# Kernel tuning notes

Measured on AMD Instinct MI355X. Metric: run time of the kernel, lower is better.

The kernel has to match this reference:

```python
import jax, jax.numpy as jnp
from jax import lax
import numpy as np

H_FEAT = 14
W_FEAT = 14
BN_EPS = 1e-5
NORM_EPS = 1e-12

def _coord_tensor():
    # Python-2 integer division as in the original repo
    c = np.zeros((H_FEAT * W_FEAT, 2), dtype=np.float32)
    for i in range(H_FEAT * W_FEAT):
        c[i, 0] = (i // W_FEAT - H_FEAT // 2) / (H_FEAT / 2.0)
        c[i, 1] = (i % W_FEAT - W_FEAT // 2) / (W_FEAT / 2.0)
    return jnp.asarray(c.reshape(1, H_FEAT, W_FEAT, 2).transpose(0, 3, 1, 2))  # [1,2,14,14]

def _l2norm(x, axis):
    n = jnp.linalg.norm(x, axis=axis, keepdims=True)
    return x / jnp.maximum(n, NORM_EPS)

def _conv2d(x, w, b, pad):
    y = lax.conv_general_dilated(x, w, (1, 1), [(pad, pad), (pad, pad)],
                                 dimension_numbers=("NCHW", "OIHW", "NCHW"))
    return y + b[None, :, None, None]

def _bn_train(x, g, b):
    m = x.mean(axis=(0, 2, 3), keepdims=True)
    v = x.var(axis=(0, 2, 3), keepdims=True)
    return (x - m) * lax.rsqrt(v + BN_EPS) * g[None, :, None, None] + b[None, :, None, None]

def _lstm_scan(emb, Wih, Whh, bih, bhh):
    # emb: [T, B, 300]; PyTorch gate order i,f,g,o
    Hdim = Whh.shape[1]
    B = emb.shape[1]
    def step(carry, x):
        h, c = carry
        gates = x @ Wih.T + h @ Whh.T + bih + bhh  # [B, 4H]
        i, f, g, o = jnp.split(gates, 4, axis=-1)
        c = jax.nn.sigmoid(f) * c + jax.nn.sigmoid(i) * jnp.tanh(g)
        h = jax.nn.sigmoid(o) * jnp.tanh(c)
        return (h, c), h
    init = (jnp.zeros((B, Hdim), emb.dtype), jnp.zeros((B, Hdim), emb.dtype))
    _, hs = lax.scan(step, init, emb)
    return hs  # [T, B, H]

def _resblock(v, coord, c1w, c1b, c2w, c2b, bng, bnb):
    B = v.shape[0]
    vin = jnp.concatenate([v, jnp.broadcast_to(coord, (B, 2, H_FEAT, W_FEAT))], axis=1)
    v1 = jax.nn.relu(_conv2d(vin, c1w, c1b, 0))
    v2 = jax.nn.relu(_bn_train(_conv2d(v1, c2w, c2b, 1), bng, bnb))
    return v2 + v1

def setup_inputs() -> dict:
    key = jax.random.key(0)
    ks = jax.random.split(key, 24)
    B, T, V, E = 128, 45, 10000, 300
    Hh = 1024
    s = 0.02
    inp = {}
    inp["que"] = jax.random.randint(ks[0], (B, T), 0, V, dtype=jnp.int64)
    inp["img"] = jax.random.normal(ks[1], (B, 1024, H_FEAT, W_FEAT), dtype=jnp.float32)
    inp["lookup"] = s * jax.random.normal(ks[2], (V + 1, E), dtype=jnp.float32)
    inp["Wih_f"] = s * jax.random.normal(ks[3], (4 * Hh, E), dtype=jnp.float32)
    inp["Whh_f"] = s * jax.random.normal(ks[4], (4 * Hh, Hh), dtype=jnp.float32)
    inp["bih_f"] = jnp.zeros((4 * Hh,), jnp.float32)
    inp["bhh_f"] = jnp.zeros((4 * Hh,), jnp.float32)
    inp["Wih_b"] = s * jax.random.normal(ks[5], (4 * Hh, E), dtype=jnp.float32)
    inp["Whh_b"] = s * jax.random.normal(ks[6], (4 * Hh, Hh), dtype=jnp.float32)
    inp["bih_b"] = jnp.zeros((4 * Hh,), jnp.float32)
    inp["bhh_b"] = jnp.zeros((4 * Hh,), jnp.float32)
    inp["conv0_w"] = s * jax.random.normal(ks[7], (128, 1026, 3, 3), dtype=jnp.float32)
    inp["conv0_b"] = jnp.zeros((128,), jnp.float32)
    inp["bn0_g"] = jnp.ones((128,), jnp.float32)
    inp["bn0_b"] = jnp.zeros((128,), jnp.float32)
    inp["r1c1_w"] = s * jax.random.normal(ks[8], (128, 130, 1, 1), dtype=jnp.float32)
    inp["r1c1_b"] = jnp.zeros((128,), jnp.float32)
    inp["r1c2_w"] = s * jax.random.normal(ks[9], (128, 128, 3, 3), dtype=jnp.float32)
    inp["r1c2_b"] = jnp.zeros((128,), jnp.float32)
    inp["r1bn_g"] = jnp.ones((128,), jnp.float32)
    inp["r1bn_b"] = jnp.zeros((128,), jnp.float32)
    inp["r2c1_w"] = s * jax.random.normal(ks[10], (128, 130, 1, 1), dtype=jnp.float32)
    inp["r2c1_b"] = jnp.zeros((128,), jnp.float32)
    inp["r2c2_w"] = s * jax.random.normal(ks[11], (128, 128, 3, 3), dtype=jnp.float32)
    inp["r2c2_b"] = jnp.zeros((128,), jnp.float32)
    inp["r2bn_g"] = jnp.ones((128,), jnp.float32)
    inp["r2bn_b"] = jnp.zeros((128,), jnp.float32)
    return inp

def reference(que, img, lookup, Wih_f, Whh_f, bih_f, bhh_f, Wih_b, Whh_b, bih_b, bhh_b,
              conv0_w, conv0_b, bn0_g, bn0_b,
              r1c1_w, r1c1_b, r1c2_w, r1c2_b, r1bn_g, r1bn_b,
              r2c1_w, r2c1_b, r2c2_w, r2c2_b, r2bn_g, r2bn_b):
    coord = _coord_tensor()
    # ---- encoder (LSTM mode) ----
    emb = lookup[que]                      # [B, T, 300]
    emb = jnp.transpose(emb, (1, 0, 2))    # [T, B, 300]
    h_f = _lstm_scan(emb, Wih_f, Whh_f, bih_f, bhh_f)
    h_b = _lstm_scan(emb[::-1], Wih_b, Whh_b, bih_b, bhh_b)[::-1]
    qenc = _l2norm(jnp.concatenate([h_f, h_b], axis=-1), axis=-1)  # [T, B, 2048]
    enc = qenc[-1]                                                  # [B, 2048]
    # ---- image branch ----
    v = _l2norm(img, axis=1)               # per-pixel L2 norm over 1024 channels
    B = v.shape[0]
    v = jnp.concatenate([v, jnp.broadcast_to(coord, (B, 2, H_FEAT, W_FEAT))], axis=1)
    v = jax.nn.relu(_bn_train(_conv2d(v, conv0_w, conv0_b, 1), bn0_g, bn0_b))
    v = _resblock(v, coord, r1c1_w, r1c1_b, r1c2_w, r1c2_b, r1bn_g, r1bn_b)
    v = _resblock(v, coord, r2c1_w, r2c1_b, r2c2_w, r2c2_b, r2bn_g, r2bn_b)
    return (enc, v)
```

## Files before the change

### kernel.cpp

```cpp
#include <hip/hip_runtime.h>
#include <math.h>

#define BB   128
#define T    45
#define E    300
#define HH   1024
#define G4   4096
#define HW   196
#define NPX  (BB*HW)
#define C0   1026
#define CM   128
#define CR   130
#define TCH  15

static __device__ __forceinline__ float sigm(float x) { return 1.f / (1.f + __expf(-x)); }

__global__ void k_embed(const int* __restrict__ que, const float* __restrict__ lookup,
                        float* __restrict__ emb) {
    int idx = blockIdx.x * 256 + threadIdx.x;
    if (idx >= T * BB * E) return;
    int e = idx % E;
    int n = idx / E;
    int b = n % BB;
    int t = n / BB;
    int q = que[b * T + t];
    emb[idx] = lookup[(size_t)q * E + e];
}

template <int BM, int BN, int TM, int TN>
__global__ __launch_bounds__(256) void k_gemm_nt(
    const float* __restrict__ A, int lda,
    const float* __restrict__ Bw, int ldb,
    const float* __restrict__ add,
    const float* __restrict__ bias,
    float* __restrict__ C, int ldc,
    int M, int N, int K, int relu) {
    constexpr int KT = 16;
    constexpr int TX = BN / TN;
    __shared__ alignas(16) float As[KT][BM + 4];
    __shared__ alignas(16) float Bs[KT][BN + 4];
    const int tid = threadIdx.x;
    const int tx = tid % TX, ty = tid / TX;
    const int r0 = blockIdx.x * BM, c0 = blockIdx.y * BN;
    float acc[TM][TN] = {};
    for (int k0 = 0; k0 < K; k0 += KT) {
#pragma unroll
        for (int l = tid; l < BM * KT; l += 256) {
            int m = l / KT, k = l % KT;
            int gm = r0 + m, gk = k0 + k;
            As[k][m] = (gm < M && gk < K) ? A[(size_t)gm * lda + gk] : 0.f;
        }
#pragma unroll
        for (int l = tid; l < BN * KT; l += 256) {
            int n = l / KT, k = l % KT;
            int gn = c0 + n, gk = k0 + k;
            Bs[k][n] = (gn < N && gk < K) ? Bw[(size_t)gn * ldb + gk] : 0.f;
        }
        __syncthreads();
#pragma unroll
        for (int k = 0; k < KT; ++k) {
            float ar[TM], br[TN];
            if constexpr ((TM & 3) == 0) {
#pragma unroll
                for (int i = 0; i < TM; i += 4) {
                    float4 v = *(const float4*)&As[k][ty * TM + i];
                    ar[i] = v.x; ar[i + 1] = v.y; ar[i + 2] = v.z; ar[i + 3] = v.w;
                }
            } else if constexpr ((TM & 1) == 0) {
#pragma unroll
                for (int i = 0; i < TM; i += 2) {
                    float2 v = *(const float2*)&As[k][ty * TM + i];
                    ar[i] = v.x; ar[i + 1] = v.y;
                }
            } else {
#pragma unroll
                for (int i = 0; i < TM; ++i) ar[i] = As[k][ty * TM + i];
            }
            if constexpr ((TN & 3) == 0) {
#pragma unroll
                for (int j = 0; j < TN; j += 4) {
                    float4 v = *(const float4*)&Bs[k][tx * TN + j];
                    br[j] = v.x; br[j + 1] = v.y; br[j + 2] = v.z; br[j + 3] = v.w;
                }
            } else if constexpr ((TN & 1) == 0) {
#pragma unroll
                for (int j = 0; j < TN; j += 2) {
                    float2 v = *(const float2*)&Bs[k][tx * TN + j];
                    br[j] = v.x; br[j + 1] = v.y;
                }
            } else {
#pragma unroll
                for (int j = 0; j < TN; ++j) br[j] = Bs[k][tx * TN + j];
            }
#pragma unroll
            for (int i = 0; i < TM; ++i)
#pragma unroll
                for (int j = 0; j < TN; ++j) acc[i][j] += ar[i] * br[j];
        }
        __syncthreads();
    }
#pragma unroll
    for (int i = 0; i < TM; ++i) {
        int gm = r0 + ty * TM + i;
        if (gm >= M) continue;
#pragma unroll
        for (int j = 0; j < TN; ++j) {
            int gn = c0 + tx * TN + j;
            if (gn >= N) continue;
            float v = acc[i][j];
            if (add) v += add[(size_t)gm * ldc + gn];
            if (bias) v += bias[gn];
            if (relu) v = fmaxf(v, 0.f);
            C[(size_t)gm * ldc + gn] = v;
        }
    }
}

__global__ void k_pack_wih(const float* __restrict__ Wih, float* __restrict__ o) {
    int idx = blockIdx.x * 256 + threadIdx.x;
    if (idx >= G4 * E) return;
    int k = idx % E;
    int n = idx / E;
    o[idx] = Wih[(size_t)((n & 3) * HH + (n >> 2)) * E + k];
}
__global__ void k_pack_whh(const float* __restrict__ Whh, float* __restrict__ o) {
    int idx = blockIdx.x * 256 + threadIdx.x;
    if (idx >= G4 * HH) return;
    int k = idx & 1023;
    int n = idx >> 10;
    o[idx] = Whh[(size_t)((n & 3) * HH + (n >> 2)) * HH + k];
}
__global__ void k_pack_b4i(const float* __restrict__ bih, const float* __restrict__ bhh,
                           float* __restrict__ out) {
    int n = blockIdx.x * 256 + threadIdx.x;
    if (n >= G4) return;
    int r = (n & 3) * HH + (n >> 2);
    out[n] = bih[r] + bhh[r];
}
__global__ void k_biasadd(const float* __restrict__ bih, const float* __restrict__ bhh,
                          float* __restrict__ out) {
    int idx = blockIdx.x * 256 + threadIdx.x;
    if (idx < G4) out[idx] = bih[idx] + bhh[idx];
}

__global__ void k_cell_plain(float* __restrict__ h, float* __restrict__ c,
                             const float* __restrict__ gx, int first) {
    int idx = blockIdx.x * 256 + threadIdx.x;
    int b = idx >> 10, j = idx & 1023;
    size_t base = (size_t)b * G4 + j;
    float gi = gx[base], gf = gx[base + HH], gg = gx[base + 2 * HH], go = gx[base + 3 * HH];
    float cp = first ? 0.f : c[idx];
    float cn = sigm(gf) * cp + sigm(gi) * tanhf(gg);
    c[idx] = cn;
    h[idx] = sigm(go) * tanhf(cn);
}

__global__ __launch_bounds__(256) void k_lstm_fused(
    const float* __restrict__ h_in, float* __restrict__ c_io,
    const float* __restrict__ gx,
    const float* __restrict__ Wpk,
    float* __restrict__ h_out, int first) {
    __shared__ alignas(16) float As[16][20];
    __shared__ alignas(16) float Bs[16][68];
    const int tid = threadIdx.x;
    const int tx = tid & 15, ty = tid >> 4;
    const int id = blockIdx.x;
    const int xcd = id & 7, slot = id >> 3;
    const int cg = xcd * 8 + (slot >> 3);
    const int rb = slot & 7;
    const int r0 = rb * 16;
    const int c0 = cg * 64;
    const int ka = tid & 15, ma = tid >> 4;
    float acc[4] = {};

    if (!first) {
        const float* hrow = h_in + (size_t)(r0 + ma) * HH + ka;
        const float* wp0 = Wpk + (size_t)(c0 + ma) * HH + ka;
        float aA = hrow[0];
        float b0A = wp0[0], b1A = wp0[16 * HH], b2A = wp0[32 * HH], b3A = wp0[48 * HH];
        float aB = hrow[16];
        float b0B = wp0[16], b1B = wp0[16 * HH + 16], b2B = wp0[32 * HH + 16],
              b3B = wp0[48 * HH + 16];
        for (int k0 = 0; k0 < HH; k0 += 16) {
            As[ka][ma] = aA;
            Bs[ka][ma] = b0A;
            Bs[ka][ma + 16] = b1A;
            Bs[ka][ma + 32] = b2A;
            Bs[ka][ma + 48] = b3A;
            __syncthreads();
            aA = aB; b0A = b0B; b1A = b1B; b2A = b2B; b3A = b3B;
            if (k0 + 32 < HH) {
                int o = k0 + 32;
                aB = hrow[o];
                b0B = wp0[o];
                b1B = wp0[16 * HH + o];
                b2B = wp0[32 * HH + o];
                b3B = wp0[48 * HH + o];
            }
#pragma unroll
            for (int k = 0; k < 16; ++k) {
                float a = As[k][ty];
                float4 b4 = *(const float4*)&Bs[k][tx * 4];
                acc[0] += a * b4.x;
                acc[1] += a * b4.y;
                acc[2] += a * b4.z;
                acc[3] += a * b4.w;
            }
            __syncthreads();
        }
    }
    const int b = r0 + ty;
    const int jj4 = c0 + tx * 4;
    const int u = jj4 >> 2;
    float4 g4 = *(const float4*)&gx[(size_t)b * G4 + jj4];
    float gi = acc[0] + g4.x;
    float gf = acc[1] + g4.y;
    float gg = acc[2] + g4.z;
    float go = acc[3] + g4.w;
    size_t ci = (size_t)b * HH + u;
    float cp = first ? 0.f : c_io[ci];
    float cn = sigm(gf) * cp + sigm(gi) * tanhf(gg);
    c_io[ci] = cn;
    h_out[ci] = sigm(go) * tanhf(cn);
}

__global__ void k_enc(const float* __restrict__ hf, const float* __restrict__ hb,
                      float* __restrict__ out) {
    int b = blockIdx.x;
    int tid = threadIdx.x;
    float vals[8];
    float ss = 0.f;
#pragma unroll
    for (int i = 0; i < 8; ++i) {
        int j = i * 256 + tid;
        float v = (j < HH) ? hf[(size_t)b * HH + j] : hb[(size_t)b * HH + (j - HH)];
        vals[i] = v;
        ss += v * v;
    }
    __shared__ float red[256];
    red[tid] = ss;
    __syncthreads();
    for (int s = 128; s > 0; s >>= 1) {
        if (tid < s) red[tid] += red[tid + s];
        __syncthreads();
    }
    float scale = 1.f / fmaxf(sqrtf(red[0]), 1e-12f);
#pragma unroll
    for (int i = 0; i < 8; ++i) out[(size_t)b * 2048 + i * 256 + tid] = vals[i] * scale;
}

__global__ void k_pixssq(const float* __restrict__ img, float* __restrict__ ssq) {
    int b = blockIdx.x >> 4;
    int cc = (blockIdx.x & 15) * 64;
    int p = threadIdx.x;
    if (p >= HW) return;
    const float* base = img + ((size_t)b * 1024 + cc) * HW + p;
    float acc = 0.f;
#pragma unroll 4
    for (int c = 0; c < 64; ++c) {
        float v = base[(size_t)c * HW];
        acc += v * v;
    }
    atomicAdd(&ssq[b * HW + p], acc);
}

__global__ void k_invn(float* __restrict__ ssq) {
    int i = blockIdx.x * 256 + threadIdx.x;
    if (i >= NPX) return;
    ssq[i] = 1.f / fmaxf(sqrtf(ssq[i]), 1e-12f);
}

__global__ void k_packB0(const float* __restrict__ w, float* __restrict__ o) {
    int idx = blockIdx.x * 256 + threadIdx.x;
    if (idx >= 16 * 9 * 1040 * 8) return;
    int oi = idx & 7;
    int r = idx >> 3;
    int c = r % 1040;
    int gt = r / 1040;
    int tap = gt % 9, ocg = gt / 9;
    o[idx] = (c < C0) ? w[((size_t)(ocg * 8 + oi) * C0 + c) * 9 + tap] : 0.f;
}
__global__ void k_packBpm(const float* __restrict__ w, float* __restrict__ o) {
    int idx = blockIdx.x * 256 + threadIdx.x;
    if (idx >= 8 * 9 * 128 * 16) return;
    int oi = idx & 15;
    int r = idx >> 4;
    int c = r % 128;
    int gt = r / 128;
    int tap = gt % 9, ocg = gt / 9;
    o[idx] = w[((size_t)(ocg * 16 + oi) * 128 + c) * 9 + tap];
}

static __device__ __forceinline__ void conv_swz3136(int id, int& g, int& ocg, int& z) {
    int s2 = (id & 7) * 392 + (id >> 3);
    g = s2 >> 5;
    int cb = s2 & 31;
    ocg = cb >> 1;
    z = cb & 1;
}
static __device__ __forceinline__ void conv_swz1568(int id, int& g, int& ocg, int& z) {
    int s2 = (id & 7) * 196 + (id >> 3);
    g = s2 >> 4;
    int cb = s2 & 15;
    ocg = cb >> 1;
    z = cb & 1;
}

__global__ __launch_bounds__(128) void k_conv0(const float* __restrict__ img,
                                               const float* __restrict__ invn,
                                               const float* __restrict__ wpk,
                                               const float* __restrict__ bias,
                                               float* __restrict__ outParts) {
    __shared__ float As[8][292];
    const int tid = threadIdx.x;
    int g, ocg, z;
    conv_swz3136(blockIdx.x, g, ocg, z);
    const int kbeg = z ? 528 : 0;
    const int kend = z ? 1032 : 528;
    float* out = outParts + (size_t)z * NPX * CM;
    const int P0 = g * 256;
    const int gp1 = P0 + tid;
    const int gp2 = gp1 + 128;
    const int p1 = gp1 % HW, p2 = gp2 % HW;
    const int y1 = p1 / 14, x1 = p1 % 14;
    const int y2 = p2 / 14, x2 = p2 % 14;

    const float* sptr[3];
    float sinv[3], scy[3], scx[3];
#pragma unroll
    for (int j = 0; j < 3; ++j) {
        int s = tid + j * 128;
        int gp = P0 - 16 + s;
        bool ok = (s < 288) && (gp >= 0) && (gp < NPX);
        int gpc = ok ? gp : 0;
        int pp = gpc % HW;
        int bi = gpc / HW;
        sptr[j] = img + ((size_t)bi * 1024) * HW + pp;
        sinv[j] = ok ? invn[gpc] : 0.f;
        scy[j] = ok ? (float)(pp / 14 - 7) * (1.f / 7.f) : 0.f;
        scx[j] = ok ? (float)(pp % 14 - 7) * (1.f / 7.f) : 0.f;
    }

    float acc0[8] = {};
    float acc1[8] = {};
    for (int k0 = kbeg; k0 < kend; k0 += 8) {
        __syncthreads();
        if (k0 != 1024) {
#pragma unroll
            for (int j = 0; j < 3; ++j) {
                int s = tid + j * 128;
                if (j < 2 || s < 292) {
                    const float* pb = sptr[j] + (size_t)k0 * HW;
                    float inv = sinv[j];
#pragma unroll
                    for (int k = 0; k < 8; ++k) As[k][s] = pb[(size_t)k * HW] * inv;
                }
            }
        } else {
#pragma unroll
            for (int j = 0; j < 3; ++j) {
                int s = tid + j * 128;
                if (j < 2 || s < 292) {
                    As[0][s] = scy[j];
                    As[1][s] = scx[j];
#pragma unroll
                    for (int k = 2; k < 8; ++k) As[k][s] = 0.f;
                }
            }
        }
        __syncthreads();
        for (int tap = 0; tap < 9; ++tap) {
            const int ky = tap / 3 - 1, kx = tap % 3 - 1;
            const int d = ky * 14 + kx;
            const int of1 = ((unsigned)(y1 + ky) < 14u && (unsigned)(x1 + kx) < 14u)
                                ? (tid + 16 + d) : 288;
            const int of2 = ((unsigned)(y2 + ky) < 14u && (unsigned)(x2 + kx) < 14u)
                                ? (tid + 144 + d) : 288;
            const float4* __restrict__ wq =
                (const float4*)wpk + ((size_t)(ocg * 9 + tap) * 1040 + k0) * 2;
#pragma unroll
            for (int k = 0; k < 8; ++k) {
                float a = As[k][of1];
                float b = As[k][of2];
                float4 w0 = wq[0], w1 = wq[1];
                wq += 2;
                acc0[0] += a * w0.x;  acc1[0] += b * w0.x;
                acc0[1] += a * w0.y;  acc1[1] += b * w0.y;
                acc0[2] += a * w0.z;  acc1[2] += b * w0.z;
                acc0[3] += a * w0.w;  acc1[3] += b * w0.w;
                acc0[4] += a * w1.x;  acc1[4] += b * w1.x;
                acc0[5] += a * w1.y;  acc1[5] += b * w1.y;
                acc0[6] += a * w1.z;  acc1[6] += b * w1.z;
                acc0[7] += a * w1.w;  acc1[7] += b * w1.w;
            }
        }
    }
    const float* bp = bias + ocg * 8;
    float* op1 = out + (size_t)gp1 * CM + ocg * 8;
    float* op2 = out + (size_t)gp2 * CM + ocg * 8;
#pragma unroll
    for (int qq = 0; qq < 2; ++qq) {
        float b0 = z ? 0.f : bp[qq * 4 + 0];
        float b1 = z ? 0.f : bp[qq * 4 + 1];
        float b2 = z ? 0.f : bp[qq * 4 + 2];
        float b3 = z ? 0.f : bp[qq * 4 + 3];
        float4 r0, r1;
        r0.x = acc0[qq * 4 + 0] + b0;  r1.x = acc1[qq * 4 + 0] + b0;
        r0.y = acc0[qq * 4 + 1] + b1;  r1.y = acc1[qq * 4 + 1] + b1;
        r0.z = acc0[qq * 4 + 2] + b2;  r1.z = acc1[qq * 4 + 2] + b2;
        r0.w = acc0[qq * 4 + 3] + b3;  r1.w = acc1[qq * 4 + 3] + b3;
        *(float4*)&op1[qq * 4] = r0;
        *(float4*)&op2[qq * 4] = r1;
    }
}

__global__ __launch_bounds__(128) void k_conv_pm(const float* __restrict__ vin,
                                                 const float* __restrict__ wpk,
                                                 const float* __restrict__ bias,
                                                 float* __restrict__ outParts) {
    __shared__ float As[8][292];
    const int tid = threadIdx.x;
    int g, ocg, z;
    conv_swz1568(blockIdx.x, g, ocg, z);
    const int kbeg = z * 64;
    float* out = outParts + (size_t)z * NPX * CM;
    const int P0 = g * 256;
    const int gp1 = P0 + tid;
    const int gp2 = gp1 + 128;
    const int p1 = gp1 % HW, p2 = gp2 % HW;
    const int y1 = p1 / 14, x1 = p1 % 14;
    const int y2 = p2 / 14, x2 = p2 % 14;

    const float* sptr[3];
    float smask[3];
#pragma unroll
    for (int j = 0; j < 3; ++j) {
        int s = tid + j * 128;
        int gp = P0 - 16 + s;
        bool ok = (s < 288) && (gp >= 0) && (gp < NPX);
        sptr[j] = vin + (size_t)(ok ? gp : 0) * CM;
        smask[j] = ok ? 1.f : 0.f;
    }

    float acc0[16] = {};
    float acc1[16] = {};
    for (int k0 = kbeg; k0 < kbeg + 64; k0 += 8) {
        __syncthreads();
#pragma unroll
        for (int j = 0; j < 3; ++j) {
            int s = tid + j * 128;
            if (j < 2 || s < 292) {
                float4 v0 = *(const float4*)&sptr[j][k0];
                float4 v1 = *(const float4*)&sptr[j][k0 + 4];
                float m = smask[j];
                As[0][s] = v0.x * m;
                As[1][s] = v0.y * m;
                As[2][s] = v0.z * m;
                As[3][s] = v0.w * m;
                As[4][s] = v1.x * m;
                As[5][s] = v1.y * m;
                As[6][s] = v1.z * m;
                As[7][s] = v1.w * m;
            }
        }
        __syncthreads();
        for (int tap = 0; tap < 9; ++tap) {
            const int ky = tap / 3 - 1, kx = tap % 3 - 1;
            const int d = ky * 14 + kx;
            const int of1 = ((unsigned)(y1 + ky) < 14u && (unsigned)(x1 + kx) < 14u)
                                ? (tid + 16 + d) : 288;
            const int of2 = ((unsigned)(y2 + ky) < 14u && (unsigned)(x2 + kx) < 14u)
                                ? (tid + 144 + d) : 288;
            const float4* __restrict__ wq =
                (const float4*)wpk + ((size_t)(ocg * 9 + tap) * 128 + k0) * 4;
#pragma unroll
            for (int k = 0; k < 8; ++k) {
                float a = As[k][of1];
                float b = As[k][of2];
                float4 w0 = wq[0], w1 = wq[1], w2 = wq[2], w3 = wq[3];
                wq += 4;
                acc0[0]  += a * w0.x;  acc1[0]  += b * w0.x;
                acc0[1]  += a * w0.y;  acc1[1]  += b * w0.y;
                acc0[2]  += a * w0.z;  acc1[2]  += b * w0.z;
                acc0[3]  += a * w0.w;  acc1[3]  += b * w0.w;
                acc0[4]  += a * w1.x;  acc1[4]  += b * w1.x;
                acc0[5]  += a * w1.y;  acc1[5]  += b * w1.y;
                acc0[6]  += a * w1.z;  acc1[6]  += b * w1.z;
                acc0[7]  += a * w1.w;  acc1[7]  += b * w1.w;
                acc0[8]  += a * w2.x;  acc1[8]  += b * w2.x;
                acc0[9]  += a * w2.y;  acc1[9]  += b * w2.y;
                acc0[10] += a * w2.z;  acc1[10] += b * w2.z;
                acc0[11] += a * w2.w;  acc1[11] += b * w2.w;
                acc0[12] += a * w3.x;  acc1[12] += b * w3.x;
                acc0[13] += a * w3.y;  acc1[13] += b * w3.y;
                acc0[14] += a * w3.z;  acc1[14] += b * w3.z;
                acc0[15] += a * w3.w;  acc1[15] += b * w3.w;
            }
        }
    }
    const float* bp = bias + ocg * 16;
    float* op1 = out + (size_t)gp1 * CM + ocg * 16;
    float* op2 = out + (size_t)gp2 * CM + ocg * 16;
#pragma unroll
    for (int qq = 0; qq < 4; ++qq) {
        float b0 = z ? 0.f : bp[qq * 4 + 0];
        float b1 = z ? 0.f : bp[qq * 4 + 1];
        float b2 = z ? 0.f : bp[qq * 4 + 2];
        float b3 = z ? 0.f : bp[qq * 4 + 3];
        float4 r0, r1;
        r0.x = acc0[qq * 4 + 0] + b0;  r1.x = acc1[qq * 4 + 0] + b0;
        r0.y = acc0[qq * 4 + 1] + b1;  r1.y = acc1[qq * 4 + 1] + b1;
        r0.z = acc0[qq * 4 + 2] + b2;  r1.z = acc1[qq * 4 + 2] + b2;
        r0.w = acc0[qq * 4 + 3] + b3;  r1.w = acc1[qq * 4 + 3] + b3;
        *(float4*)&op1[qq * 4] = r0;
        *(float4*)&op2[qq * 4] = r1;
    }
}

__global__ void k_bnstats(const float* __restrict__ xa, const float* __restrict__ xb,
                          float* __restrict__ stats) {
    int r0 = blockIdx.x * 224;
    int c = threadIdx.x & 127, rh = threadIdx.x >> 7;
    float s = 0.f, ss = 0.f;
    for (int r = r0 + rh; r < r0 + 224; r += 2) {
        float v = xa[(size_t)r * CM + c] + xb[(size_t)r * CM + c];
        s += v;
        ss += v * v;
    }
    __shared__ float rs[256], rss[256];
    rs[threadIdx.x] = s;
    rss[threadIdx.x] = ss;
    __syncthreads();
    if (threadIdx.x < 128) {
        s = rs[threadIdx.x] + rs[threadIdx.x + 128];
        ss = rss[threadIdx.x] + rss[threadIdx.x + 128];
        atomicAdd(&stats[c], s);
        atomicAdd(&stats[128 + c], ss);
    }
}

__global__ void k_apply_cat(const float* __restrict__ xa, const float* __restrict__ xb,
                            const float* __restrict__ stats,
                            const float* __restrict__ gg, const float* __restrict__ bb,
                            const float* __restrict__ addv, float* __restrict__ vinr) {
    int idx = blockIdx.x * 256 + threadIdx.x;
    if (idx >= NPX * CM) return;
    int c = idx & 127;
    int p = idx >> 7;
    float mean = stats[c] * (1.f / (float)NPX);
    float var = stats[128 + c] * (1.f / (float)NPX) - mean * mean;
    float sc = gg[c] * rsqrtf(var + 1e-5f);
    float sh = bb[c] - mean * sc;
    float v = fmaxf((xa[idx] + xb[idx]) * sc + sh, 0.f);
    if (addv) v += addv[idx];
    vinr[(size_t)p * CR + c] = v;
    if (c < 2) {
        int pp = p % HW;
        float cv = (c == 0) ? (float)(pp / 14 - 7) * (1.f / 7.f)
                            : (float)(pp % 14 - 7) * (1.f / 7.f);
        vinr[(size_t)p * CR + 128 + c] = cv;
    }
}

__global__ void k_final(const float* __restrict__ xa, const float* __restrict__ xb,
                        const float* __restrict__ stats,
                        const float* __restrict__ gg, const float* __restrict__ bb,
                        const float* __restrict__ addv, float* __restrict__ outv) {
    int idx = blockIdx.x * 256 + threadIdx.x;
    if (idx >= NPX * CM) return;
    int p = idx % HW;
    int o = (idx / HW) & 127;
    int b = idx / (HW * CM);
    float mean = stats[o] * (1.f / (float)NPX);
    float var = stats[128 + o] * (1.f / (float)NPX) - mean * mean;
    float sc = gg[o] * rsqrtf(var + 1e-5f);
    float sh = bb[o] - mean * sc;
    size_t pm = ((size_t)b * HW + p) * CM + o;
    outv[idx] = fmaxf((xa[pm] + xb[pm]) * sc + sh, 0.f) + addv[pm];
}

extern "C" void kernel_launch(void* const* d_in, const int* in_sizes, int n_in,
                              void* d_out, int out_size, void* d_ws, size_t ws_size,
                              hipStream_t stream) {
    const int* que = (const int*)d_in[0];
    const float* img = (const float*)d_in[1];
    const float* lookup = (const float*)d_in[2];
    const float* Wih_f = (const float*)d_in[3];
    const float* Whh_f = (const float*)d_in[4];
    const float* bih_f = (const float*)d_in[5];
    const float* bhh_f = (const float*)d_in[6];
    const float* Wih_b = (const float*)d_in[7];
    const float* bih_b = (const float*)d_in[9];
    const float* bhh_b = (const float*)d_in[10];
    const float* conv0_w = (const float*)d_in[11];
    const float* conv0_b = (const float*)d_in[12];
    const float* bn0_g = (const float*)d_in[13];
    const float* bn0_b = (const float*)d_in[14];
    const float* r1c1_w = (const float*)d_in[15];
    const float* r1c1_b = (const float*)d_in[16];
    const float* r1c2_w = (const float*)d_in[17];
    const float* r1c2_b = (const float*)d_in[18];
    const float* r1bn_g = (const float*)d_in[19];
    const float* r1bn_b = (const float*)d_in[20];
    const float* r2c1_w = (const float*)d_in[21];
    const float* r2c1_b = (const float*)d_in[22];
    const float* r2c2_w = (const float*)d_in[23];
    const float* r2c2_b = (const float*)d_in[24];
    const float* r2bn_g = (const float*)d_in[25];
    const float* r2bn_b = (const float*)d_in[26];
    float* out = (float*)d_out;

    float* ws = (float*)d_ws;
    float* emb = ws;
    float* Xg = emb + 1728000;
    float* WihPk = Xg + 7864320;
    float* WhhPk = WihPk + 1228800;
    float* b4i = WhhPk + 4194304;
    float* b4b = b4i + 4096;
    float* Xb = b4b + 4096;
    float* hA = Xb + 524288;
    float* hB = hA + 131072;
    float* cbuf = hB + 131072;
    float* hbb = cbuf + 131072;
    size_t lstm_end = (size_t)(hbb + 131072 - ws);
    float* invn = ws;
    float* wpk0 = invn + 25088;
    float* wpk1 = wpk0 + 1198080;
    float* wpk2 = wpk1 + 147456;
    float* xa = wpk2 + 147456;
    float* xb = xa + 3211264;
    float* vinr = xb + 3211264;
    float* v1 = vinr + 3261440;
    float* stats = v1 + 3211264;
    size_t img_end = (size_t)(stats + 256 - ws);
    size_t need = (lstm_end > img_end ? lstm_end : img_end) * 4;
    if (ws_size < need) return;

    auto cdiv = [](int a, int b) { return (a + b - 1) / b; };
    const size_t BG = (size_t)BB * G4;

    k_embed<<<cdiv(T * BB * E, 256), 256, 0, stream>>>(que, lookup, emb);
    k_pack_wih<<<cdiv(G4 * E, 256), 256, 0, stream>>>(Wih_f, WihPk);
    k_pack_whh<<<cdiv(G4 * HH, 256), 256, 0, stream>>>(Whh_f, WhhPk);
    k_pack_b4i<<<16, 256, 0, stream>>>(bih_f, bhh_f, b4i);
    k_biasadd<<<16, 256, 0, stream>>>(bih_b, bhh_b, b4b);
    k_gemm_nt<64, 64, 4, 4><<<dim3(2, 64), 256, 0, stream>>>(
        emb + (size_t)(T - 1) * BB * E, E, Wih_b, E, nullptr, b4b, Xb, G4, BB, G4, E, 0);
    k_cell_plain<<<512, 256, 0, stream>>>(hbb, cbuf, Xb, 1);
    float* hp = hA;
    float* hq = hB;
    float* hlast = hA;
    for (int ch = 0; ch < 3; ++ch) {
        int t0 = ch * TCH;
        k_gemm_nt<64, 128, 4, 8><<<dim3(30, 32), 256, 0, stream>>>(
            emb + (size_t)t0 * BB * E, E, WihPk, E, nullptr, b4i, Xg, G4,
            TCH * BB, G4, E, 0);
        for (int s = 0; s < TCH; ++s) {
            int t = t0 + s;
            k_lstm_fused<<<512, 256, 0, stream>>>(
                hq, cbuf, Xg + (size_t)s * BG, WhhPk, hp, (t == 0) ? 1 : 0);
            hlast = hp;
            float* tmp = hp; hp = hq; hq = tmp;
        }
    }
    k_enc<<<128, 256, 0, stream>>>(hlast, hbb, out);

    hipMemsetAsync(invn, 0, NPX * 4, stream);
    k_pixssq<<<BB * 16, 256, 0, stream>>>(img, invn);
    k_invn<<<cdiv(NPX, 256), 256, 0, stream>>>(invn);
    k_packB0<<<cdiv(16 * 9 * 1040 * 8, 256), 256, 0, stream>>>(conv0_w, wpk0);
    k_packBpm<<<cdiv(8 * 9 * 128 * 16, 256), 256, 0, stream>>>(r1c2_w, wpk1);
    k_packBpm<<<cdiv(8 * 9 * 128 * 16, 256), 256, 0, stream>>>(r2c2_w, wpk2);

    k_conv0<<<3136, 128, 0, stream>>>(img, invn, wpk0, conv0_b, xa);
    hipMemsetAsync(stats, 0, 256 * 4, stream);
    k_bnstats<<<112, 256, 0, stream>>>(xa, xb, stats);
    k_apply_cat<<<cdiv(NPX * CM, 256), 256, 0, stream>>>(xa, xb, stats, bn0_g, bn0_b,
                                                         nullptr, vinr);

    k_gemm_nt<128, 64, 8, 4><<<dim3(196, 2), 256, 0, stream>>>(
        vinr, CR, r1c1_w, CR, nullptr, r1c1_b, v1, CM, NPX, CM, CR, 1);
    k_conv_pm<<<1568, 128, 0, stream>>>(v1, wpk1, r1c2_b, xa);
    hipMemsetAsync(stats, 0, 256 * 4, stream);
    k_bnstats<<<112, 256, 0, stream>>>(xa, xb, stats);
    k_apply_cat<<<cdiv(NPX * CM, 256), 256, 0, stream>>>(xa, xb, stats, r1bn_g, r1bn_b,
                                                         v1, vinr);

    k_gemm_nt<128, 64, 8, 4><<<dim3(196, 2), 256, 0, stream>>>(
        vinr, CR, r2c1_w, CR, nullptr, r2c1_b, v1, CM, NPX, CM, CR, 1);
    k_conv_pm<<<1568, 128, 0, stream>>>(v1, wpk2, r2c2_b, xa);
    hipMemsetAsync(stats, 0, 256 * 4, stream);
    k_bnstats<<<112, 256, 0, stream>>>(xa, xb, stats);
    k_final<<<cdiv(NPX * CM, 256), 256, 0, stream>>>(xa, xb, stats, r2bn_g, r2bn_b,
                                                     v1, out + (size_t)BB * 2048);
}
```

Measured before the change: 3.506 ms.

## Run LSTM recurrence chunks as persistent cooperative kernels with grid sync

Replaces the 45 per-timestep LSTM kernel launches with three cooperative launches, each running 15 steps and separating them with a grid-wide barrier. The aim is to remove per-step launch overhead and scheduling gaps in the serial recurrence. The h ping-pong buffers are now chosen by timestep parity, and a fallback to per-step launches is kept in case the cooperative launch fails. Separately, the inverse-norm kernel is removed and its reciprocal square root is folded into conv0's load of the sum of squares. The risks are grid-sync cost on MI355X and the need for all 512 blocks to be co-resident.

```diff
diff --git a/kernel.cpp b/kernel.cpp
--- a/kernel.cpp
+++ b/kernel.cpp
@@ -1,5 +1,8 @@
 #include <hip/hip_runtime.h>
+#include <hip/hip_cooperative_groups.h>
 #include <math.h>
+
+namespace cg = cooperative_groups;
 
 #define BB   128
 #define T    45
@@ -155,73 +158,93 @@
     h[idx] = sigm(go) * tanhf(cn);
 }
 
-__global__ __launch_bounds__(256) void k_lstm_fused(
-    const float* __restrict__ h_in, float* __restrict__ c_io,
-    const float* __restrict__ gx,
-    const float* __restrict__ Wpk,
-    float* __restrict__ h_out, int first) {
+template <bool MULTI>
+static __device__ __forceinline__ void lstm_body(
+    const float* __restrict__ Xg, const float* __restrict__ Wpk,
+    float* __restrict__ hA, float* __restrict__ hB, float* __restrict__ cb,
+    int t0, int nsteps, int first_chunk) {
     __shared__ alignas(16) float As[16][20];
     __shared__ alignas(16) float Bs[16][68];
     const int tid = threadIdx.x;
     const int tx = tid & 15, ty = tid >> 4;
     const int id = blockIdx.x;
     const int xcd = id & 7, slot = id >> 3;
-    const int cg = xcd * 8 + (slot >> 3);
+    const int cg2 = xcd * 8 + (slot >> 3);
     const int rb = slot & 7;
     const int r0 = rb * 16;
-    const int c0 = cg * 64;
+    const int c0 = cg2 * 64;
     const int ka = tid & 15, ma = tid >> 4;
-    float acc[4] = {};
-
-    if (!first) {
-        const float* hrow = h_in + (size_t)(r0 + ma) * HH + ka;
-        const float* wp0 = Wpk + (size_t)(c0 + ma) * HH + ka;
-        float aA = hrow[0];
-        float b0A = wp0[0], b1A = wp0[16 * HH], b2A = wp0[32 * HH], b3A = wp0[48 * HH];
-        float aB = hrow[16];
-        float b0B = wp0[16], b1B = wp0[16 * HH + 16], b2B = wp0[32 * HH + 16],
-              b3B = wp0[48 * HH + 16];
-        for (int k0 = 0; k0 < HH; k0 += 16) {
-            As[ka][ma] = aA;
-            Bs[ka][ma] = b0A;
-            Bs[ka][ma + 16] = b1A;
-            Bs[ka][ma + 32] = b2A;
-            Bs[ka][ma + 48] = b3A;
-            __syncthreads();
-            aA = aB; b0A = b0B; b1A = b1B; b2A = b2B; b3A = b3B;
-            if (k0 + 32 < HH) {
-                int o = k0 + 32;
-                aB = hrow[o];
-                b0B = wp0[o];
-                b1B = wp0[16 * HH + o];
-                b2B = wp0[32 * HH + o];
-                b3B = wp0[48 * HH + o];
-            }
-#pragma unroll
-            for (int k = 0; k < 16; ++k) {
-                float a = As[k][ty];
-                float4 b4 = *(const float4*)&Bs[k][tx * 4];
-                acc[0] += a * b4.x;
-                acc[1] += a * b4.y;
-                acc[2] += a * b4.z;
-                acc[3] += a * b4.w;
-            }
-            __syncthreads();
-        }
-    }
     const int b = r0 + ty;
     const int jj4 = c0 + tx * 4;
     const int u = jj4 >> 2;
-    float4 g4 = *(const float4*)&gx[(size_t)b * G4 + jj4];
-    float gi = acc[0] + g4.x;
-    float gf = acc[1] + g4.y;
-    float gg = acc[2] + g4.z;
-    float go = acc[3] + g4.w;
-    size_t ci = (size_t)b * HH + u;
-    float cp = first ? 0.f : c_io[ci];
-    float cn = sigm(gf) * cp + sigm(gi) * tanhf(gg);
-    c_io[ci] = cn;
-    h_out[ci] = sigm(go) * tanhf(cn);
+    const size_t ci = (size_t)b * HH + u;
+    const float* wp0 = Wpk + (size_t)(c0 + ma) * HH + ka;
+
+    for (int s = 0; s < nsteps; ++s) {
+        const int t = t0 + s;
+        const int first = (first_chunk && s == 0) ? 1 : 0;
+        float acc[4] = {};
+        if (!first) {
+            const float* h_in = (t & 1) ? hA : hB;
+            const float* hrow = h_in + (size_t)(r0 + ma) * HH + ka;
+            float aA = hrow[0];
+            float b0A = wp0[0], b1A = wp0[16 * HH], b2A = wp0[32 * HH], b3A = wp0[48 * HH];
+            float aB = hrow[16];
+            float b0B = wp0[16], b1B = wp0[16 * HH + 16], b2B = wp0[32 * HH + 16],
+                  b3B = wp0[48 * HH + 16];
+            for (int k0 = 0; k0 < HH; k0 += 16) {
+                As[ka][ma] = aA;
+                Bs[ka][ma] = b0A;
+                Bs[ka][ma + 16] = b1A;
+                Bs[ka][ma + 32] = b2A;
+                Bs[ka][ma + 48] = b3A;
+                __syncthreads();
+                aA = aB; b0A = b0B; b1A = b1B; b2A = b2B; b3A = b3B;
+                if (k0 + 32 < HH) {
+                    int o = k0 + 32;
+                    aB = hrow[o];
+                    b0B = wp0[o];
+                    b1B = wp0[16 * HH + o];
+                    b2B = wp0[32 * HH + o];
+                    b3B = wp0[48 * HH + o];
+                }
+#pragma unroll
+                for (int k = 0; k < 16; ++k) {
+                    float a = As[k][ty];
+                    float4 b4 = *(const float4*)&Bs[k][tx * 4];
+                    acc[0] += a * b4.x;
+                    acc[1] += a * b4.y;
+                    acc[2] += a * b4.z;
+                    acc[3] += a * b4.w;
+                }
+                __syncthreads();
+            }
+        }
+        float* h_out = (t & 1) ? hB : hA;
+        float4 g4 = *(const float4*)&Xg[(size_t)s * BB * G4 + (size_t)b * G4 + jj4];
+        float gi = acc[0] + g4.x;
+        float gf = acc[1] + g4.y;
+        float gg = acc[2] + g4.z;
+        float go = acc[3] + g4.w;
+        float cp = first ? 0.f : cb[ci];
+        float cn = sigm(gf) * cp + sigm(gi) * tanhf(gg);
+        cb[ci] = cn;
+        h_out[ci] = sigm(go) * tanhf(cn);
+        if constexpr (MULTI) cg::this_grid().sync();
+    }
+}
+
+__global__ __launch_bounds__(256) void k_lstm_coop(
+    const float* __restrict__ Xg, const float* __restrict__ Wpk,
+    float* __restrict__ hA, float* __restrict__ hB, float* __restrict__ cb,
+    int t0, int nsteps, int first_chunk) {
+    lstm_body<true>(Xg, Wpk, hA, hB, cb, t0, nsteps, first_chunk);
+}
+__global__ __launch_bounds__(256) void k_lstm_fused(
+    const float* __restrict__ Xg, const float* __restrict__ Wpk,
+    float* __restrict__ hA, float* __restrict__ hB, float* __restrict__ cb,
+    int t, int first) {
+    lstm_body<false>(Xg, Wpk, hA, hB, cb, t, 1, first);
 }
 
 __global__ void k_enc(const float* __restrict__ hf, const float* __restrict__ hb,
@@ -264,12 +287,6 @@
     atomicAdd(&ssq[b * HW + p], acc);
 }
 
-__global__ void k_invn(float* __restrict__ ssq) {
-    int i = blockIdx.x * 256 + threadIdx.x;
-    if (i >= NPX) return;
-    ssq[i] = 1.f / fmaxf(sqrtf(ssq[i]), 1e-12f);
-}
-
 __global__ void k_packB0(const float* __restrict__ w, float* __restrict__ o) {
     int idx = blockIdx.x * 256 + threadIdx.x;
     if (idx >= 16 * 9 * 1040 * 8) return;
@@ -307,7 +324,7 @@
 }
 
 __global__ __launch_bounds__(128) void k_conv0(const float* __restrict__ img,
-                                               const float* __restrict__ invn,
+                                               const float* __restrict__ ssq,
                                                const float* __restrict__ wpk,
                                                const float* __restrict__ bias,
                                                float* __restrict__ outParts) {
@@ -336,7 +353,7 @@
         int pp = gpc % HW;
         int bi = gpc / HW;
         sptr[j] = img + ((size_t)bi * 1024) * HW + pp;
-        sinv[j] = ok ? invn[gpc] : 0.f;
+        sinv[j] = ok ? (1.f / fmaxf(sqrtf(ssq[gpc]), 1e-12f)) : 0.f;
         scy[j] = ok ? (float)(pp / 14 - 7) * (1.f / 7.f) : 0.f;
         scx[j] = ok ? (float)(pp % 14 - 7) * (1.f / 7.f) : 0.f;
     }
@@ -623,8 +640,8 @@
     float* cbuf = hB + 131072;
     float* hbb = cbuf + 131072;
     size_t lstm_end = (size_t)(hbb + 131072 - ws);
-    float* invn = ws;
-    float* wpk0 = invn + 25088;
+    float* ssq = ws;
+    float* wpk0 = ssq + 25088;
     float* wpk1 = wpk0 + 1198080;
     float* wpk2 = wpk1 + 147456;
     float* xa = wpk2 + 147456;
@@ -647,32 +664,38 @@
     k_gemm_nt<64, 64, 4, 4><<<dim3(2, 64), 256, 0, stream>>>(
         emb + (size_t)(T - 1) * BB * E, E, Wih_b, E, nullptr, b4b, Xb, G4, BB, G4, E, 0);
     k_cell_plain<<<512, 256, 0, stream>>>(hbb, cbuf, Xb, 1);
-    float* hp = hA;
-    float* hq = hB;
-    float* hlast = hA;
+    int coop_ok = 1;
     for (int ch = 0; ch < 3; ++ch) {
         int t0 = ch * TCH;
         k_gemm_nt<64, 128, 4, 8><<<dim3(30, 32), 256, 0, stream>>>(
             emb + (size_t)t0 * BB * E, E, WihPk, E, nullptr, b4i, Xg, G4,
             TCH * BB, G4, E, 0);
-        for (int s = 0; s < TCH; ++s) {
-            int t = t0 + s;
-            k_lstm_fused<<<512, 256, 0, stream>>>(
-                hq, cbuf, Xg + (size_t)s * BG, WhhPk, hp, (t == 0) ? 1 : 0);
-            hlast = hp;
-            float* tmp = hp; hp = hq; hq = tmp;
-        }
-    }
-    k_enc<<<128, 256, 0, stream>>>(hlast, hbb, out);
-
-    hipMemsetAsync(invn, 0, NPX * 4, stream);
-    k_pixssq<<<BB * 16, 256, 0, stream>>>(img, invn);
-    k_invn<<<cdiv(NPX, 256), 256, 0, stream>>>(invn);
+        if (coop_ok) {
+            int ns = TCH, fr = (ch == 0) ? 1 : 0;
+            void* args[] = {(void*)&Xg, (void*)&WhhPk, (void*)&hA, (void*)&hB,
+                            (void*)&cbuf, (void*)&t0, (void*)&ns, (void*)&fr};
+            hipError_t e = hipLaunchCooperativeKernel(
+                reinterpret_cast<void*>(k_lstm_coop), dim3(512), dim3(256, 1, 1),
+                args, 0, stream);
+            if (e != hipSuccess) coop_ok = 0;
+        }
+        if (!coop_ok) {
+            for (int s = 0; s < TCH; ++s) {
+                int t = t0 + s;
+                k_lstm_fused<<<512, 256, 0, stream>>>(
+                    Xg + (size_t)s * BG, WhhPk, hA, hB, cbuf, t, (t == 0) ? 1 : 0);
+            }
+        }
+    }
+    k_enc<<<128, 256, 0, stream>>>(hA, hbb, out);
+
+    hipMemsetAsync(ssq, 0, NPX * 4, stream);
+    k_pixssq<<<BB * 16, 256, 0, stream>>>(img, ssq);
     k_packB0<<<cdiv(16 * 9 * 1040 * 8, 256), 256, 0, stream>>>(conv0_w, wpk0);
     k_packBpm<<<cdiv(8 * 9 * 128 * 16, 256), 256, 0, stream>>>(r1c2_w, wpk1);
     k_packBpm<<<cdiv(8 * 9 * 128 * 16, 256), 256, 0, stream>>>(r2c2_w, wpk2);
 
-    k_conv0<<<3136, 128, 0, stream>>>(img, invn, wpk0, conv0_b, xa);
+    k_conv0<<<3136, 128, 0, stream>>>(img, ssq, wpk0, conv0_b, xa);
     hipMemsetAsync(stats, 0, 256 * 4, stream);
     k_bnstats<<<112, 256, 0, stream>>>(xa, xb, stats);
     k_apply_cat<<<cdiv(NPX * CM, 256), 256, 0, stream>>>(xa, xb, stats, bn0_g, bn0_b,
```

New measurement: 6.074 ms. 73.2% more time.
